# Kernel optimization log

Hardware: AMD Instinct MI355X
Metric: run time of the kernel (lower is better)

## Reference

```python
import jax, jax.numpy as jnp
import numpy as np

GAMMA = 1.0
INPUT_DIM = 512
NUM_CENTERS = 4096
BATCH = 16384


def setup_inputs() -> dict:
    key = jax.random.key(0)
    kx, kc = jax.random.split(key)
    x = jax.random.normal(kx, (BATCH, INPUT_DIM), dtype=jnp.float32)
    centers = jax.random.normal(kc, (NUM_CENTERS, INPUT_DIM), dtype=jnp.float32)
    return {"x": x, "centers": centers}


def reference(x, centers):
    x_sq = jnp.sum(x * x, axis=-1, keepdims=True)            # [B, 1]
    c_sq = jnp.sum(centers * centers, axis=-1)               # [C]
    cross = jnp.einsum("bd,cd->bc", x, centers)              # [B, C]
    dist_sq = x_sq - 2.0 * cross + c_sq[None, :]
    return jnp.exp(-GAMMA * dist_sq)
```

## Files before the change

kernel.cpp:

```cpp
#include <hip/hip_runtime.h>
#include <stdint.h>

#define M_DIM 16384
#define N_DIM 4096
#define K_DIM 512

#define BM 128
#define BN 128
#define BK 64
#define LDS_STRIDE 72

typedef __bf16 bf16x8 __attribute__((ext_vector_type(8)));
typedef float f32x4 __attribute__((ext_vector_type(4)));

__device__ __forceinline__ unsigned pack_bf16(float lo, float hi) {
    return __builtin_amdgcn_perm(__float_as_uint(hi), __float_as_uint(lo), 0x07060302u);
}

__global__ void row_norms_kernel(const float* __restrict__ src,
                                 float* __restrict__ dst, int nrows) {
    int wave = threadIdx.x >> 6;
    int lane = threadIdx.x & 63;
    int row = blockIdx.x * 4 + wave;
    if (row >= nrows) return;
    const float4* p = (const float4*)(src + (size_t)row * K_DIM);
    float4 a = p[lane];
    float4 b = p[lane + 64];
    float s = a.x*a.x + a.y*a.y + a.z*a.z + a.w*a.w
            + b.x*b.x + b.y*b.y + b.z*b.z + b.w*b.w;
    #pragma unroll
    for (int off = 32; off > 0; off >>= 1) s += __shfl_down(s, off, 64);
    if (lane == 0) dst[row] = s;
}

__global__ __launch_bounds__(256)
void rbf_mfma_kernel(const float* __restrict__ X, const float* __restrict__ C,
                     const float* __restrict__ xsq, const float* __restrict__ csq,
                     float* __restrict__ out) {
    __shared__ uint16_t As[BM * LDS_STRIDE];
    __shared__ uint16_t Bs[BN * LDS_STRIDE];

    const int tid  = threadIdx.x;
    const int lane = tid & 63;
    const int wave = tid >> 6;
    const int wm = (wave >> 1) * 64;
    const int wn = (wave & 1) * 64;
    const int q   = lane >> 4;
    const int c16 = lane & 15;

    const int bn = (blockIdx.x & 31) * BN;
    const int bm = (blockIdx.x >> 5) * BM;

    const int srow  = tid >> 3;
    const int skoff = (tid & 7) * 8;

    f32x4 acc[4][4] = {};

    const float* Abase = X + (size_t)(bm + srow) * K_DIM + skoff;
    const float* Bbase = C + (size_t)(bn + srow) * K_DIM + skoff;

    for (int k0 = 0; k0 < K_DIM; k0 += BK) {
        #pragma unroll
        for (int p = 0; p < 4; ++p) {
            const float4* ap = (const float4*)(Abase + (size_t)(32 * p) * K_DIM + k0);
            float4 f0 = ap[0], f1 = ap[1];
            uint4 ua;
            ua.x = pack_bf16(f0.x, f0.y);
            ua.y = pack_bf16(f0.z, f0.w);
            ua.z = pack_bf16(f1.x, f1.y);
            ua.w = pack_bf16(f1.z, f1.w);
            *(uint4*)&As[(srow + 32 * p) * LDS_STRIDE + skoff] = ua;

            const float4* bp = (const float4*)(Bbase + (size_t)(32 * p) * K_DIM + k0);
            float4 g0 = bp[0], g1 = bp[1];
            uint4 ub;
            ub.x = pack_bf16(g0.x, g0.y);
            ub.y = pack_bf16(g0.z, g0.w);
            ub.z = pack_bf16(g1.x, g1.y);
            ub.w = pack_bf16(g1.z, g1.w);
            *(uint4*)&Bs[(srow + 32 * p) * LDS_STRIDE + skoff] = ub;
        }
        __syncthreads();

        #pragma unroll
        for (int ks = 0; ks < 2; ++ks) {
            bf16x8 af[4], bfr[4];
            #pragma unroll
            for (int i = 0; i < 4; ++i)
                af[i] = *(const bf16x8*)&As[(wm + 16 * i + c16) * LDS_STRIDE + ks * 32 + q * 8];
            #pragma unroll
            for (int j = 0; j < 4; ++j)
                bfr[j] = *(const bf16x8*)&Bs[(wn + 16 * j + c16) * LDS_STRIDE + ks * 32 + q * 8];
            #pragma unroll
            for (int i = 0; i < 4; ++i)
                #pragma unroll
                for (int j = 0; j < 4; ++j)
                    acc[i][j] = __builtin_amdgcn_mfma_f32_16x16x32_bf16(
                        af[i], bfr[j], acc[i][j], 0, 0, 0);
        }
        __syncthreads();
    }

    float cs[4];
    #pragma unroll
    for (int j = 0; j < 4; ++j) cs[j] = csq[bn + wn + 16 * j + c16];

    #pragma unroll
    for (int i = 0; i < 4; ++i) {
        #pragma unroll
        for (int r = 0; r < 4; ++r) {
            int m = bm + wm + 16 * i + q * 4 + r;
            float xs = xsq[m];
            float* orow = out + (size_t)m * N_DIM + bn + wn;
            #pragma unroll
            for (int j = 0; j < 4; ++j) {
                float dist = xs - 2.0f * acc[i][j][r] + cs[j];
                orow[16 * j + c16] = __expf(-dist);
            }
        }
    }
}

extern "C" void kernel_launch(void* const* d_in, const int* in_sizes, int n_in,
                              void* d_out, int out_size, void* d_ws, size_t ws_size,
                              hipStream_t stream) {
    const float* X = (const float*)d_in[0];
    const float* C = (const float*)d_in[1];
    float* out = (float*)d_out;
    float* xsq = (float*)d_ws;
    float* csq = xsq + M_DIM;

    row_norms_kernel<<<M_DIM / 4, 256, 0, stream>>>(X, xsq, M_DIM);
    row_norms_kernel<<<N_DIM / 4, 256, 0, stream>>>(C, csq, N_DIM);
    rbf_mfma_kernel<<<(M_DIM / BM) * (N_DIM / BN), 256, 0, stream>>>(X, C, xsq, csq, out);
}
```

Before: 362.6 us.

## Pre-convert inputs to bf16 and stream tiles via direct global-to-LDS loads

The norm kernels now also write bf16 copies of X and C to workspace. The GEMM then loads those bf16 tiles straight into a XOR-swizzled LDS layout with global_load_lds, so it no longer reloads fp32 and converts inside the main loop. The tile widens to 128x256 and uses 32x32x16 MFMA, with launch bounds set for 2 blocks per SM. This cuts GEMM global traffic and conversion ALU work, at the cost of an extra workspace write and read and no double buffering.

```diff
diff --git a/kernel.cpp b/kernel.cpp
--- a/kernel.cpp
+++ b/kernel.cpp
@@ -4,98 +4,110 @@
 #define M_DIM 16384
 #define N_DIM 4096
 #define K_DIM 512
+#define KB2 1024
 
 #define BM 128
-#define BN 128
+#define BN 256
 #define BK 64
-#define LDS_STRIDE 72
 
 typedef __bf16 bf16x8 __attribute__((ext_vector_type(8)));
-typedef float f32x4 __attribute__((ext_vector_type(4)));
+typedef float f32x16 __attribute__((ext_vector_type(16)));
+
+typedef __attribute__((address_space(3))) uint32_t lds_u32_t;
+typedef const __attribute__((address_space(1))) uint32_t glob_u32_t;
+
+__device__ __forceinline__ void gload16(const void* g, void* l) {
+    __builtin_amdgcn_global_load_lds((glob_u32_t*)g, (lds_u32_t*)l, 16, 0, 0);
+}
 
 __device__ __forceinline__ unsigned pack_bf16(float lo, float hi) {
     return __builtin_amdgcn_perm(__float_as_uint(hi), __float_as_uint(lo), 0x07060302u);
 }
 
-__global__ void row_norms_kernel(const float* __restrict__ src,
-                                 float* __restrict__ dst, int nrows) {
-    int wave = threadIdx.x >> 6;
-    int lane = threadIdx.x & 63;
-    int row = blockIdx.x * 4 + wave;
+__global__ __launch_bounds__(256)
+void convert_norm_kernel(const float* __restrict__ src, uint16_t* __restrict__ dst,
+                         float* __restrict__ norms, int nrows) {
+    const int wave = threadIdx.x >> 6;
+    const int lane = threadIdx.x & 63;
+    const int row = blockIdx.x * 4 + wave;
     if (row >= nrows) return;
-    const float4* p = (const float4*)(src + (size_t)row * K_DIM);
-    float4 a = p[lane];
-    float4 b = p[lane + 64];
+    const float4* p = (const float4*)(src + (size_t)row * K_DIM) + lane * 2;
+    float4 a = p[0], b = p[1];
+    uint4 u;
+    u.x = pack_bf16(a.x, a.y);
+    u.y = pack_bf16(a.z, a.w);
+    u.z = pack_bf16(b.x, b.y);
+    u.w = pack_bf16(b.z, b.w);
+    *(uint4*)(dst + (size_t)row * K_DIM + lane * 8) = u;
     float s = a.x*a.x + a.y*a.y + a.z*a.z + a.w*a.w
             + b.x*b.x + b.y*b.y + b.z*b.z + b.w*b.w;
     #pragma unroll
     for (int off = 32; off > 0; off >>= 1) s += __shfl_down(s, off, 64);
-    if (lane == 0) dst[row] = s;
+    if (lane == 0) norms[row] = s;
 }
 
-__global__ __launch_bounds__(256)
-void rbf_mfma_kernel(const float* __restrict__ X, const float* __restrict__ C,
+__global__ __launch_bounds__(256, 2)
+void rbf_mfma_kernel(const uint16_t* __restrict__ Abf, const uint16_t* __restrict__ Bbf,
                      const float* __restrict__ xsq, const float* __restrict__ csq,
                      float* __restrict__ out) {
-    __shared__ uint16_t As[BM * LDS_STRIDE];
-    __shared__ uint16_t Bs[BN * LDS_STRIDE];
+    __shared__ uint16_t As[BM * BK];
+    __shared__ uint16_t Bs[BN * BK];
 
     const int tid  = threadIdx.x;
     const int lane = tid & 63;
     const int wave = tid >> 6;
+    const int l31  = lane & 31;
+    const int half = lane >> 5;
+    const int l7   = lane & 7;
+
+    const int bn = (blockIdx.x & 15) * BN;
+    const int bm = (blockIdx.x >> 4) * BM;
+
     const int wm = (wave >> 1) * 64;
-    const int wn = (wave & 1) * 64;
-    const int q   = lane >> 4;
-    const int c16 = lane & 15;
+    const int wn = (wave & 1) * 128;
 
-    const int bn = (blockIdx.x & 31) * BN;
-    const int bm = (blockIdx.x >> 5) * BM;
+    const int srow   = tid >> 3;
+    const int schunk = (tid & 7) ^ (srow & 7);
+    const size_t soff = (size_t)srow * KB2 + (size_t)schunk * 16;
 
-    const int srow  = tid >> 3;
-    const int skoff = (tid & 7) * 8;
+    const uint8_t* pA = (const uint8_t*)Abf + (size_t)bm * KB2 + soff;
+    const uint8_t* pB = (const uint8_t*)Bbf + (size_t)bn * KB2 + soff;
+    uint8_t* AsB = (uint8_t*)As;
+    uint8_t* BsB = (uint8_t*)Bs;
 
-    f32x4 acc[4][4] = {};
+    const uint16_t* Arow = As + (wm + l31) * BK;
+    const uint16_t* Brow = Bs + (wn + l31) * BK;
+    int slot[4];
+    #pragma unroll
+    for (int ks = 0; ks < 4; ++ks) slot[ks] = (((ks * 2 + half) ^ l7) * 8);
 
-    const float* Abase = X + (size_t)(bm + srow) * K_DIM + skoff;
-    const float* Bbase = C + (size_t)(bn + srow) * K_DIM + skoff;
+    f32x16 acc[2][4] = {};
 
-    for (int k0 = 0; k0 < K_DIM; k0 += BK) {
+    for (int kk = 0; kk < K_DIM / BK; ++kk) {
         #pragma unroll
-        for (int p = 0; p < 4; ++p) {
-            const float4* ap = (const float4*)(Abase + (size_t)(32 * p) * K_DIM + k0);
-            float4 f0 = ap[0], f1 = ap[1];
-            uint4 ua;
-            ua.x = pack_bf16(f0.x, f0.y);
-            ua.y = pack_bf16(f0.z, f0.w);
-            ua.z = pack_bf16(f1.x, f1.y);
-            ua.w = pack_bf16(f1.z, f1.w);
-            *(uint4*)&As[(srow + 32 * p) * LDS_STRIDE + skoff] = ua;
-
-            const float4* bp = (const float4*)(Bbase + (size_t)(32 * p) * K_DIM + k0);
-            float4 g0 = bp[0], g1 = bp[1];
-            uint4 ub;
-            ub.x = pack_bf16(g0.x, g0.y);
-            ub.y = pack_bf16(g0.z, g0.w);
-            ub.z = pack_bf16(g1.x, g1.y);
-            ub.w = pack_bf16(g1.z, g1.w);
-            *(uint4*)&Bs[(srow + 32 * p) * LDS_STRIDE + skoff] = ub;
-        }
+        for (int t = 0; t < 4; ++t)
+            gload16(pA + (size_t)t * 32 * KB2, AsB + t * 4096 + wave * 1024);
+        #pragma unroll
+        for (int t = 0; t < 8; ++t)
+            gload16(pB + (size_t)t * 32 * KB2, BsB + t * 4096 + wave * 1024);
+        pA += BK * 2;
+        pB += BK * 2;
         __syncthreads();
 
         #pragma unroll
-        for (int ks = 0; ks < 2; ++ks) {
-            bf16x8 af[4], bfr[4];
+        for (int ks = 0; ks < 4; ++ks) {
+            bf16x8 af[2], bfr[4];
             #pragma unroll
-            for (int i = 0; i < 4; ++i)
-                af[i] = *(const bf16x8*)&As[(wm + 16 * i + c16) * LDS_STRIDE + ks * 32 + q * 8];
+            for (int i = 0; i < 2; ++i)
+                af[i] = *(const bf16x8*)(Arow + i * 32 * BK + slot[ks]);
             #pragma unroll
             for (int j = 0; j < 4; ++j)
-                bfr[j] = *(const bf16x8*)&Bs[(wn + 16 * j + c16) * LDS_STRIDE + ks * 32 + q * 8];
+                bfr[j] = *(const bf16x8*)(Brow + j * 32 * BK + slot[ks]);
             #pragma unroll
-            for (int i = 0; i < 4; ++i)
+            for (int i = 0; i < 2; ++i)
                 #pragma unroll
                 for (int j = 0; j < 4; ++j)
-                    acc[i][j] = __builtin_amdgcn_mfma_f32_16x16x32_bf16(
+                    acc[i][j] = __builtin_amdgcn_mfma_f32_32x32x16_bf16(
                         af[i], bfr[j], acc[i][j], 0, 0, 0);
         }
         __syncthreads();
@@ -103,19 +115,19 @@
 
     float cs[4];
     #pragma unroll
-    for (int j = 0; j < 4; ++j) cs[j] = csq[bn + wn + 16 * j + c16];
+    for (int j = 0; j < 4; ++j) cs[j] = csq[bn + wn + 32 * j + l31];
 
     #pragma unroll
-    for (int i = 0; i < 4; ++i) {
+    for (int i = 0; i < 2; ++i) {
         #pragma unroll
-        for (int r = 0; r < 4; ++r) {
-            int m = bm + wm + 16 * i + q * 4 + r;
-            float xs = xsq[m];
-            float* orow = out + (size_t)m * N_DIM + bn + wn;
+        for (int r = 0; r < 16; ++r) {
+            const int gm = bm + wm + 32 * i + 4 * half + (r & 3) + 8 * (r >> 2);
+            const float xs = xsq[gm];
+            float* orow = out + (size_t)gm * N_DIM + bn + wn;
             #pragma unroll
             for (int j = 0; j < 4; ++j) {
-                float dist = xs - 2.0f * acc[i][j][r] + cs[j];
-                orow[16 * j + c16] = __expf(-dist);
+                float d = xs - 2.0f * acc[i][j][r] + cs[j];
+                orow[32 * j + l31] = __expf(-d);
             }
         }
     }
@@ -127,10 +139,13 @@
     const float* X = (const float*)d_in[0];
     const float* C = (const float*)d_in[1];
     float* out = (float*)d_out;
-    float* xsq = (float*)d_ws;
+
+    uint16_t* Xbf = (uint16_t*)d_ws;
+    uint16_t* Cbf = Xbf + (size_t)M_DIM * K_DIM;
+    float* xsq = (float*)(Cbf + (size_t)N_DIM * K_DIM);
     float* csq = xsq + M_DIM;
 
-    row_norms_kernel<<<M_DIM / 4, 256, 0, stream>>>(X, xsq, M_DIM);
-    row_norms_kernel<<<N_DIM / 4, 256, 0, stream>>>(C, csq, N_DIM);
-    rbf_mfma_kernel<<<(M_DIM / BM) * (N_DIM / BN), 256, 0, stream>>>(X, C, xsq, csq, out);
+    convert_norm_kernel<<<M_DIM / 4, 256, 0, stream>>>(X, Xbf, xsq, M_DIM);
+    convert_norm_kernel<<<N_DIM / 4, 256, 0, stream>>>(C, Cbf, csq, N_DIM);
+    rbf_mfma_kernel<<<(M_DIM / BM) * (N_DIM / BN), 256, 0, stream>>>(Xbf, Cbf, xsq, csq, out);
 }
```

Result: faster. 343.7 us (-5.2%).
